# Performance work log

Hardware: AMD Instinct MI355X
Metric: run time of the kernel (lower is better)

## Reference

```python
import jax, jax.numpy as jnp
import numpy as np

HEAD_DIM = 256
V_DIM = 256
HIDDEN = 1024
SCALE_BASE = 512
GAMMA = 0.96875
BATCH, SEQ = 4, 4096


def _dup_interleave(m):
    # (L, d/2) -> (L, d), duplicating each column consecutively
    return jnp.repeat(m, 2, axis=-1)


def _rotate_every_two(x):
    x1 = x[..., ::2]
    x2 = x[..., 1::2]
    return jnp.stack([-x2, x1], axis=-1).reshape(x.shape)


def _xpos(x, downscale=False):
    # x: (B, L, head_dim); offset=0 path of XPOS.forward
    B, L, Dh = x.shape
    half = Dh // 2
    scale_buf = (jnp.arange(0, Dh, 2, dtype=jnp.float32) + 0.4 * Dh) / (1.4 * Dh)  # (half,)
    pos = jnpp = jnp.arange(L, dtype=jnp.float32)
    scale = scale_buf[None, :] ** (pos / SCALE_BASE)[:, None]  # (L, half)
    inv_freq = 1.0 / (10000.0 ** (jnp.arange(half, dtype=jnp.float32) / half))
    sinusoid = pos[:, None] * inv_freq[None, :]  # (L, half)
    sin, cos = jnp.sin(sinusoid), jnp.cos(sinusoid)
    if downscale:
        scale = 1.0 / scale
    cos_s = _dup_interleave(cos * scale)  # (L, Dh)
    sin_s = _dup_interleave(sin * scale)
    return x * cos_s[None] + _rotate_every_two(x) * sin_s[None]


def _decay_matrix(L):
    n = jnp.arange(L)[:, None]
    m = jnp.arange(L)[None, :]
    mask = n >= m
    expo = jnp.where(mask, n - m, 0).astype(jnp.float32)
    return jnp.where(mask, GAMMA ** expo, 0.0)  # (L, L)


def setup_inputs() -> dict:
    key = jax.random.key(0)
    k1, k2, k3, k4 = jax.random.split(key, 4)
    X = jax.random.normal(k1, (BATCH, SEQ, HIDDEN), dtype=jnp.float32)
    W_Q = jax.random.normal(k2, (HIDDEN, HEAD_DIM), dtype=jnp.float32) / HIDDEN
    W_K = jax.random.normal(k3, (HIDDEN, HEAD_DIM), dtype=jnp.float32) / HIDDEN
    W_V = jax.random.normal(k4, (HIDDEN, V_DIM), dtype=jnp.float32) / HIDDEN
    return {"X": X, "W_Q": W_Q, "W_K": W_K, "W_V": W_V}


def reference(X, W_Q, W_K, W_V):
    L = X.shape[1]
    Q = _xpos(X @ W_Q)                      # (B, L, Dh)
    K = _xpos(X @ W_K, downscale=True)      # (B, L, Dh)
    V = X @ W_V                             # (B, L, Dv)
    D = _decay_matrix(L)                    # (L, L)
    ret = jnp.einsum('bqd,bkd->bqk', Q, K) * D[None]  # (B, L, L)
    return ret @ V                          # (B, L, Dv)
```

## Files before the change

### kernel.cpp

```cpp
#include <hip/hip_runtime.h>
#include <hip/hip_bf16.h>
#include <cstdint>
#include <cstddef>

#define L_SEQ 4096
#define BATCH_N 4
#define HID 1024
#define DH 256
#define LOG2_GAMMA (-0.045803689613124953f)
#define INV_GAMMA32 (2.7620582f)

typedef __attribute__((ext_vector_type(8))) short short8;
typedef __attribute__((ext_vector_type(4))) float floatx4;

__device__ __forceinline__ unsigned short f2bf(float f) {
    union { float f; unsigned int u; } v; v.f = f;
    unsigned int r = (v.u + 0x7FFFu + ((v.u >> 16) & 1u)) >> 16;
    return (unsigned short)r;
}

__device__ __forceinline__ void async_copy16(const unsigned short* gsrc,
                                             unsigned short* lds) {
    __builtin_amdgcn_global_load_lds(
        (const __attribute__((address_space(1))) unsigned int*)gsrc,
        (__attribute__((address_space(3))) unsigned int*)lds, 16, 0, 0);
}

__global__ __launch_bounds__(256) void prep_kernel(
    const float* __restrict__ X, unsigned short* __restrict__ Xb,
    float2* __restrict__ tabQ, float2* __restrict__ tabK,
    const float* __restrict__ WQ, const float* __restrict__ WK,
    const float* __restrict__ WV, unsigned short* __restrict__ Wt,
    float* __restrict__ O)
{
    __shared__ float Ts[64][68];
    const int bid = blockIdx.x;
    const int t   = threadIdx.x;

    if (bid < 16384) {
        const int i = (bid * 256 + t) * 4;
        const float4 v = *(const float4*)&X[i];
        ushort4 p;
        p.x = f2bf(v.x); p.y = f2bf(v.y); p.z = f2bf(v.z); p.w = f2bf(v.w);
        *(ushort4*)&Xb[i] = p;
    } else if (bid < 18432) {
        const int gid = (bid - 16384) * 256 + t;
        const int i2  = gid >> 12;
        const int pos = gid & (L_SEQ - 1);
        const float e   = (float)pos * (1.0f / 512.0f);
        const float sb  = ((float)(2 * i2) + 102.4f) * (1.0f / 358.4f);
        const float scQ = exp2f(log2f(sb) * e);
        const float scK = 1.0f / scQ;
        const float invf = exp2f(-13.287712379549449f *
                                 ((float)i2 * (1.0f / 128.0f)));
        float s, c;
        sincosf((float)pos * invf, &s, &c);
        tabQ[gid] = make_float2(c * scQ, s * scQ);
        tabK[gid] = make_float2(c * scK, s * scK);
    } else if (bid < 18624) {
        const int idx = bid - 18432;
        const int n0 = (idx % 12) * 64;
        const int k0 = (idx / 12) * 64;
        const int seg = n0 >> 8;
        const float* __restrict__ W = (seg == 0) ? WQ : (seg == 1) ? WK : WV;
        const int nl0 = n0 & 255;

        const int r  = t >> 4;
        const int c4 = (t & 15) * 4;
        #pragma unroll
        for (int i = 0; i < 4; ++i) {
            const int kk = r + i * 16;
            const float4 v = *(const float4*)&W[(size_t)(k0 + kk) * DH + nl0 + c4];
            Ts[c4 + 0][kk] = v.x;
            Ts[c4 + 1][kk] = v.y;
            Ts[c4 + 2][kk] = v.z;
            Ts[c4 + 3][kk] = v.w;
        }
        __syncthreads();
        const int rn = t >> 3;
        const int c8 = (t & 7) * 8;
        #pragma unroll
        for (int i = 0; i < 2; ++i) {
            const int rr = rn + i * 32;
            ushort4 p0, p1;
            p0.x = f2bf(Ts[rr][c8 + 0]); p0.y = f2bf(Ts[rr][c8 + 1]);
            p0.z = f2bf(Ts[rr][c8 + 2]); p0.w = f2bf(Ts[rr][c8 + 3]);
            p1.x = f2bf(Ts[rr][c8 + 4]); p1.y = f2bf(Ts[rr][c8 + 5]);
            p1.z = f2bf(Ts[rr][c8 + 6]); p1.w = f2bf(Ts[rr][c8 + 7]);
            unsigned short* dst = &Wt[(size_t)(n0 + rr) * HID + k0 + c8];
            *(ushort4*)dst       = p0;
            *(ushort4*)(dst + 4) = p1;
        }
    } else {
        const int gid = (bid - 18624) * 256 + t;
        float4 z = (float4){0.f, 0.f, 0.f, 0.f};
        float4* dst = (float4*)O + (size_t)gid * 8;
        #pragma unroll
        for (int i = 0; i < 8; ++i) dst[i] = z;
    }
}

__global__ __launch_bounds__(256) void gemm_qkv_kernel(
    const unsigned short* __restrict__ Wt,
    const unsigned short* __restrict__ Xb,
    const float2* __restrict__ tabQ,
    const float2* __restrict__ tabK,
    unsigned short* __restrict__ Qo,
    unsigned short* __restrict__ Ko,
    unsigned short* __restrict__ VtG)
{
    __shared__ unsigned short Wa[3][128][32];
    __shared__ unsigned short Xs[3][128][32];

    const int dblk = blockIdx.x;
    const int xcd  = dblk & 7;
    const int sq   = dblk >> 3;
    const int by   = xcd * 16 + sq / 6;
    const int bx   = sq % 6;

    const int n0 = bx * 128;
    const int p0 = by * 128;
    const int t    = threadIdx.x;
    const int w    = t >> 6;
    const int lane = t & 63;
    const int quad = lane >> 4;
    const int l16  = lane & 15;
    const int wn   = (w & 1) * 64;
    const int wp   = (w >> 1) * 64;

    const int r16 = lane & 15;
    const int kq8 = (lane >> 4) * 8;

    floatx4 acc[4][4];
    #pragma unroll
    for (int i = 0; i < 4; ++i)
        #pragma unroll
        for (int j = 0; j < 4; ++j) acc[i][j] = (floatx4){0.f, 0.f, 0.f, 0.f};

    const int NT = HID / 32;

    auto stage = [&](int buf, int kt) {
        const int k0 = kt * 32;
        #pragma unroll
        for (int is = 0; is < 2; ++is) {
            const unsigned short* ga =
                &Wt[(size_t)(n0 + w * 32 + is * 16 + r16) * HID + k0 + kq8];
            const unsigned short* gb =
                &Xb[(size_t)(p0 + w * 32 + is * 16 + r16) * HID + k0 + kq8];
            async_copy16(ga, &Wa[buf][w * 32 + is * 16][0]);
            async_copy16(gb, &Xs[buf][w * 32 + is * 16][0]);
        }
    };

    stage(0, 0);
    stage(1, 1);

    for (int kt = 0; kt < NT; ++kt) {
        const int buf = kt % 3;
        if (kt + 1 < NT)
            asm volatile("s_waitcnt vmcnt(4)" ::: "memory");
        else
            asm volatile("s_waitcnt vmcnt(0)" ::: "memory");
        __builtin_amdgcn_s_barrier();

        if (kt + 2 < NT) stage((kt + 2) % 3, kt + 2);

        const char* wbp = (const char*)&Wa[buf][0][0];
        const char* xbp = (const char*)&Xs[buf][0][0];
        short8 af[4], bfv[4];
        #pragma unroll
        for (int nt = 0; nt < 4; ++nt)
            af[nt] = *(const short8*)(wbp + ((w & 1) * 4 + nt) * 1024 +
                                      quad * 256 + l16 * 16);
        #pragma unroll
        for (int pt = 0; pt < 4; ++pt)
            bfv[pt] = *(const short8*)(xbp + ((w >> 1) * 4 + pt) * 1024 +
                                       quad * 256 + l16 * 16);
        #pragma unroll
        for (int nt = 0; nt < 4; ++nt)
            #pragma unroll
            for (int pt = 0; pt < 4; ++pt)
                acc[nt][pt] = __builtin_amdgcn_mfma_f32_16x16x32_bf16(
                    af[nt], bfv[pt], acc[nt][pt], 0, 0, 0);
    }

    const int seg = n0 >> 8;
    const float2* __restrict__ tab = (seg == 1) ? tabK : tabQ;
    #pragma unroll
    for (int nt = 0; nt < 4; ++nt) {
        const int nfeat = n0 + wn + nt * 16 + quad * 4;
        const int d0 = nfeat & 255;
        #pragma unroll
        for (int pt = 0; pt < 4; ++pt) {
            const int pg  = p0 + wp + pt * 16 + l16;
            const int b   = pg >> 12;
            const int pos = pg & (L_SEQ - 1);
            if (seg == 2) {
                #pragma unroll
                for (int g = 0; g < 4; ++g)
                    VtG[(((size_t)(b * 256 + d0 + g)) << 12) + pos] =
                        f2bf(acc[nt][pt][g]);
            } else {
                float res[4];
                #pragma unroll
                for (int h = 0; h < 4; h += 2) {
                    const int i2 = (d0 + h) >> 1;
                    const float2 tc = tab[(i2 << 12) + pos];
                    const float cs = tc.x, ss = tc.y;
                    const float xe = acc[nt][pt][h], xo = acc[nt][pt][h + 1];
                    res[h]     = xe * cs - xo * ss;
                    res[h + 1] = xo * cs + xe * ss;
                }
                ushort4 pk;
                pk.x = f2bf(res[0]); pk.y = f2bf(res[1]);
                pk.z = f2bf(res[2]); pk.w = f2bf(res[3]);
                unsigned short* orow =
                    ((seg == 0) ? Qo : Ko) + (size_t)pg * DH + d0;
                *(ushort4*)orow = pk;
            }
        }
    }
}

__global__ __launch_bounds__(256) void retention_kernel(
    const unsigned short* __restrict__ Q,
    const unsigned short* __restrict__ K,
    const unsigned short* __restrict__ VtG,
    float* __restrict__ O)
{
    __shared__ short Ks[32][264];
    __shared__ short Vt[256][40];

    const int dblk = blockIdx.x;
    const int xcd  = dblk & 7;
    const int sq   = dblk >> 3;
    const int qt   = xcd * 8 + (sq & 7);
    const int b    = (sq >> 3) & 3;
    const int z    = sq >> 5;

    const int t  = threadIdx.x;
    const int q0 = qt * 64;

    const int w    = t >> 6;
    const int lane = t & 63;
    const int quad = lane >> 4;
    const int l16  = lane & 15;
    const int w16  = w * 16;

    const size_t rbase = (size_t)b * L_SEQ * DH;
    const size_t vbase = ((size_t)b * DH) << 12;

    int kst = q0 - 512; if (kst < 0) kst = 0;
    const int half32 = ((q0 + 64 - kst) >> 6) << 5;
    const int kbeg = kst + (z ? half32 : 0);
    const int kfin = z ? (q0 + 64) : (kst + half32);

    short8 qf[8];
    {
        const unsigned short* qsrc = Q + rbase + (size_t)(q0 + w16 + l16) * DH;
        #pragma unroll
        for (int dd = 0; dd < 8; ++dd)
            qf[dd] = *(const short8*)&qsrc[dd * 32 + quad * 8];
    }

    int   dint[8];
    float dec[8];
    #pragma unroll
    for (int nt = 0; nt < 2; ++nt)
        #pragma unroll
        for (int g = 0; g < 4; ++g) {
            const int idx = nt * 4 + g;
            dint[idx] = (q0 + w16 + l16) - (kbeg + nt * 16 + quad * 4 + g);
            dec[idx]  = exp2f((float)dint[idx] * LOG2_GAMMA);
        }

    floatx4 o[16];
    #pragma unroll
    for (int f = 0; f < 16; ++f) o[f] = (floatx4){0.f, 0.f, 0.f, 0.f};

    const int s0   = (quad & 1) * 2;
    const int idxA = (s0 * 16 + l16) * 4;
    const int idxB = idxA + 64;
    const bool lo  = (quad < 2);

    for (int k0 = kbeg; k0 < kfin; k0 += 32) {
        __syncthreads();
        {
            const unsigned short* src = K + rbase + (size_t)k0 * DH;
            #pragma unroll
            for (int i = 0; i < 4; ++i) {
                const int row = i * 8 + (t >> 5);
                const int col = (t & 31) * 8;
                *(uint4*)&Ks[row][col] = *(const uint4*)&src[row * DH + col];
            }
        }
        {
            const int c0   = t >> 2;
            const int koff = (t & 3) * 8;
            #pragma unroll
            for (int i = 0; i < 4; ++i) {
                const int c = c0 + 64 * i;
                *(uint4*)&Vt[c][koff] =
                    *(const uint4*)&VtG[vbase + ((size_t)c << 12) + k0 + koff];
            }
        }
        __syncthreads();

        floatx4 sA0 = (floatx4){0.f, 0.f, 0.f, 0.f};
        floatx4 sA1 = (floatx4){0.f, 0.f, 0.f, 0.f};
        floatx4 sB0 = (floatx4){0.f, 0.f, 0.f, 0.f};
        floatx4 sB1 = (floatx4){0.f, 0.f, 0.f, 0.f};
        #pragma unroll
        for (int dd = 0; dd < 4; ++dd) {
            const short8 k0f = *(const short8*)&Ks[l16][dd * 32 + quad * 8];
            const short8 k1f = *(const short8*)&Ks[16 + l16][dd * 32 + quad * 8];
            const short8 k0g = *(const short8*)&Ks[l16][(dd + 4) * 32 + quad * 8];
            const short8 k1g = *(const short8*)&Ks[16 + l16][(dd + 4) * 32 + quad * 8];
            sA0 = __builtin_amdgcn_mfma_f32_16x16x32_bf16(k0f, qf[dd], sA0, 0, 0, 0);
            sA1 = __builtin_amdgcn_mfma_f32_16x16x32_bf16(k1f, qf[dd], sA1, 0, 0, 0);
            sB0 = __builtin_amdgcn_mfma_f32_16x16x32_bf16(k0g, qf[dd + 4], sB0, 0, 0, 0);
            sB1 = __builtin_amdgcn_mfma_f32_16x16x32_bf16(k1g, qf[dd + 4], sB1, 0, 0, 0);
        }
        const floatx4 sv0 = sA0 + sB0;
        const floatx4 sv1 = sA1 + sB1;

        unsigned int pk01[2], pk23[2];
        #pragma unroll
        for (int nt = 0; nt < 2; ++nt) {
            const floatx4 sv = nt ? sv1 : sv0;
            float pv[4];
            #pragma unroll
            for (int g = 0; g < 4; ++g) {
                const int idx = nt * 4 + g;
                pv[g] = (dint[idx] >= 0) ? sv[g] * dec[idx] : 0.0f;
            }
            pk01[nt] = ((unsigned int)f2bf(pv[1]) << 16) | (unsigned int)f2bf(pv[0]);
            pk23[nt] = ((unsigned int)f2bf(pv[3]) << 16) | (unsigned int)f2bf(pv[2]);
        }
        #pragma unroll
        for (int i = 0; i < 8; ++i) { dint[i] -= 32; dec[i] *= INV_GAMMA32; }

        const int a01_0 = __builtin_amdgcn_ds_bpermute(idxA, (int)pk01[0]);
        const int a01_1 = __builtin_amdgcn_ds_bpermute(idxA, (int)pk01[1]);
        const int a23_0 = __builtin_amdgcn_ds_bpermute(idxA, (int)pk23[0]);
        const int a23_1 = __builtin_amdgcn_ds_bpermute(idxA, (int)pk23[1]);
        const int b01_0 = __builtin_amdgcn_ds_bpermute(idxB, (int)pk01[0]);
        const int b01_1 = __builtin_amdgcn_ds_bpermute(idxB, (int)pk01[1]);
        const int b23_0 = __builtin_amdgcn_ds_bpermute(idxB, (int)pk23[0]);
        const int b23_1 = __builtin_amdgcn_ds_bpermute(idxB, (int)pk23[1]);
        union { int u[4]; short8 s8; } af;
        af.u[0] = lo ? a01_0 : a01_1;
        af.u[1] = lo ? a23_0 : a23_1;
        af.u[2] = lo ? b01_0 : b01_1;
        af.u[3] = lo ? b23_0 : b23_1;

        #pragma unroll
        for (int f = 0; f < 16; ++f) {
            const short8 bfr = *(const short8*)&Vt[f * 16 + l16][quad * 8];
            o[f] = __builtin_amdgcn_mfma_f32_16x16x32_bf16(af.s8, bfr, o[f], 0, 0, 0);
        }
    }

    #pragma unroll
    for (int f = 0; f < 16; ++f) {
        #pragma unroll
        for (int g = 0; g < 4; ++g) {
            const int qpos = q0 + w16 + quad * 4 + g;
            atomicAdd(&O[rbase + (size_t)qpos * DH + f * 16 + l16], o[f][g]);
        }
    }
}

extern "C" void kernel_launch(void* const* d_in, const int* in_sizes, int n_in,
                              void* d_out, int out_size, void* d_ws, size_t ws_size,
                              hipStream_t stream)
{
    const float* X  = (const float*)d_in[0];
    const float* WQ = (const float*)d_in[1];
    const float* WK = (const float*)d_in[2];
    const float* WV = (const float*)d_in[3];
    float* out = (float*)d_out;

    const size_t per = (size_t)BATCH_N * L_SEQ * DH;
    unsigned short* Qw  = (unsigned short*)d_ws;
    unsigned short* Kw  = Qw + per;
    unsigned short* Vtw = Kw + per;
    unsigned short* Xbw = Vtw + per;
    unsigned short* Wtw = Xbw + (size_t)16384 * HID;
    float2* tabQ = (float2*)(Wtw + 786432);
    float2* tabK = tabQ + (size_t)128 * L_SEQ;

    prep_kernel<<<19136, 256, 0, stream>>>(X, Xbw, tabQ, tabK,
                                           WQ, WK, WV, Wtw, out);

    gemm_qkv_kernel<<<768, 256, 0, stream>>>(Wtw, Xbw, tabQ, tabK, Qw, Kw, Vtw);

    retention_kernel<<<512, 256, 0, stream>>>(Qw, Kw, Vtw, out);
}
```

Baseline: 213.3 us.

## Split retention work over value-dim halves and deepen QKV GEMM K-tiles with swizzle

The retention kernel now splits the value dimension between the two z-blocks instead of splitting the key range. Each block writes its 128 output columns directly, which removes the output zero-fill in prep and all fp32 atomics. The price is that each block recomputes the full QK^T scores for its key range. The QKV GEMM moves from a 3-stage 32-wide K pipeline to a 2-stage 64-wide one with an XOR-swizzled LDS layout, plus an extra barrier before the next stage is issued. This is meant to cut LDS bank conflicts and loop overhead, at some cost in load/compute overlap.

```diff
diff --git a/kernel.cpp b/kernel.cpp
--- a/kernel.cpp
+++ b/kernel.cpp
@@ -30,8 +30,7 @@
     const float* __restrict__ X, unsigned short* __restrict__ Xb,
     float2* __restrict__ tabQ, float2* __restrict__ tabK,
     const float* __restrict__ WQ, const float* __restrict__ WK,
-    const float* __restrict__ WV, unsigned short* __restrict__ Wt,
-    float* __restrict__ O)
+    const float* __restrict__ WV, unsigned short* __restrict__ Wt)
 {
     __shared__ float Ts[64][68];
     const int bid = blockIdx.x;
@@ -57,7 +56,7 @@
         sincosf((float)pos * invf, &s, &c);
         tabQ[gid] = make_float2(c * scQ, s * scQ);
         tabK[gid] = make_float2(c * scK, s * scK);
-    } else if (bid < 18624) {
+    } else {
         const int idx = bid - 18432;
         const int n0 = (idx % 12) * 64;
         const int k0 = (idx / 12) * 64;
@@ -91,12 +90,6 @@
             *(ushort4*)dst       = p0;
             *(ushort4*)(dst + 4) = p1;
         }
-    } else {
-        const int gid = (bid - 18624) * 256 + t;
-        float4 z = (float4){0.f, 0.f, 0.f, 0.f};
-        float4* dst = (float4*)O + (size_t)gid * 8;
-        #pragma unroll
-        for (int i = 0; i < 8; ++i) dst[i] = z;
     }
 }
 
@@ -109,8 +102,8 @@
     unsigned short* __restrict__ Ko,
     unsigned short* __restrict__ VtG)
 {
-    __shared__ unsigned short Wa[3][128][32];
-    __shared__ unsigned short Xs[3][128][32];
+    __shared__ unsigned short Wa[2][128][64];
+    __shared__ unsigned short Xs[2][128][64];
 
     const int dblk = blockIdx.x;
     const int xcd  = dblk & 7;
@@ -128,60 +121,69 @@
     const int wn   = (w & 1) * 64;
     const int wp   = (w >> 1) * 64;
 
-    const int r16 = lane & 15;
-    const int kq8 = (lane >> 4) * 8;
-
     floatx4 acc[4][4];
     #pragma unroll
     for (int i = 0; i < 4; ++i)
         #pragma unroll
         for (int j = 0; j < 4; ++j) acc[i][j] = (floatx4){0.f, 0.f, 0.f, 0.f};
 
-    const int NT = HID / 32;
-
+    const int NT = HID / 64;
+
+    const int g8 = lane >> 3;
+    const int pc = lane & 7;
+    const int sc = (pc ^ g8) * 8;
     auto stage = [&](int buf, int kt) {
-        const int k0 = kt * 32;
-        #pragma unroll
-        for (int is = 0; is < 2; ++is) {
+        const int k0 = kt * 64;
+        #pragma unroll
+        for (int is = 0; is < 4; ++is) {
+            const int gr = w * 8 + is * 32 + g8;
             const unsigned short* ga =
-                &Wt[(size_t)(n0 + w * 32 + is * 16 + r16) * HID + k0 + kq8];
+                &Wt[(size_t)(n0 + gr) * HID + k0 + sc];
             const unsigned short* gb =
-                &Xb[(size_t)(p0 + w * 32 + is * 16 + r16) * HID + k0 + kq8];
-            async_copy16(ga, &Wa[buf][w * 32 + is * 16][0]);
-            async_copy16(gb, &Xs[buf][w * 32 + is * 16][0]);
+                &Xb[(size_t)(p0 + gr) * HID + k0 + sc];
+            async_copy16(ga, &Wa[buf][is * 32 + w * 8][0]);
+            async_copy16(gb, &Xs[buf][is * 32 + w * 8][0]);
         }
     };
 
     stage(0, 0);
     stage(1, 1);
 
+    const int xr = l16 & 7;
+
     for (int kt = 0; kt < NT; ++kt) {
-        const int buf = kt % 3;
+        const int buf = kt & 1;
         if (kt + 1 < NT)
-            asm volatile("s_waitcnt vmcnt(4)" ::: "memory");
+            asm volatile("s_waitcnt vmcnt(8)" ::: "memory");
         else
             asm volatile("s_waitcnt vmcnt(0)" ::: "memory");
         __builtin_amdgcn_s_barrier();
 
-        if (kt + 2 < NT) stage((kt + 2) % 3, kt + 2);
-
         const char* wbp = (const char*)&Wa[buf][0][0];
         const char* xbp = (const char*)&Xs[buf][0][0];
-        short8 af[4], bfv[4];
-        #pragma unroll
-        for (int nt = 0; nt < 4; ++nt)
-            af[nt] = *(const short8*)(wbp + ((w & 1) * 4 + nt) * 1024 +
-                                      quad * 256 + l16 * 16);
-        #pragma unroll
-        for (int pt = 0; pt < 4; ++pt)
-            bfv[pt] = *(const short8*)(xbp + ((w >> 1) * 4 + pt) * 1024 +
-                                       quad * 256 + l16 * 16);
-        #pragma unroll
-        for (int nt = 0; nt < 4; ++nt)
+        short8 af[2][4], bfv[2][4];
+        #pragma unroll
+        for (int kk = 0; kk < 2; ++kk) {
+            const int pk = (((kk << 2) | quad) ^ xr) << 4;
             #pragma unroll
-            for (int pt = 0; pt < 4; ++pt)
-                acc[nt][pt] = __builtin_amdgcn_mfma_f32_16x16x32_bf16(
-                    af[nt], bfv[pt], acc[nt][pt], 0, 0, 0);
+            for (int nt = 0; nt < 4; ++nt) {
+                af[kk][nt]  = *(const short8*)(wbp + (wn + nt * 16 + l16) * 128 + pk);
+                bfv[kk][nt] = *(const short8*)(xbp + (wp + nt * 16 + l16) * 128 + pk);
+            }
+        }
+        asm volatile("s_waitcnt lgkmcnt(0)" ::: "memory");
+        __builtin_amdgcn_s_barrier();
+
+        if (kt + 2 < NT) stage(buf, kt + 2);
+
+        #pragma unroll
+        for (int kk = 0; kk < 2; ++kk)
+            #pragma unroll
+            for (int nt = 0; nt < 4; ++nt)
+                #pragma unroll
+                for (int pt = 0; pt < 4; ++pt)
+                    acc[nt][pt] = __builtin_amdgcn_mfma_f32_16x16x32_bf16(
+                        af[kk][nt], bfv[kk][pt], acc[nt][pt], 0, 0, 0);
     }
 
     const int seg = n0 >> 8;
@@ -229,7 +231,7 @@
     float* __restrict__ O)
 {
     __shared__ short Ks[32][264];
-    __shared__ short Vt[256][40];
+    __shared__ short Vt[128][40];
 
     const int dblk = blockIdx.x;
     const int xcd  = dblk & 7;
@@ -251,9 +253,7 @@
     const size_t vbase = ((size_t)b * DH) << 12;
 
     int kst = q0 - 512; if (kst < 0) kst = 0;
-    const int half32 = ((q0 + 64 - kst) >> 6) << 5;
-    const int kbeg = kst + (z ? half32 : 0);
-    const int kfin = z ? (q0 + 64) : (kst + half32);
+    const int kfin = q0 + 64;
 
     short8 qf[8];
     {
@@ -270,20 +270,20 @@
         #pragma unroll
         for (int g = 0; g < 4; ++g) {
             const int idx = nt * 4 + g;
-            dint[idx] = (q0 + w16 + l16) - (kbeg + nt * 16 + quad * 4 + g);
+            dint[idx] = (q0 + w16 + l16) - (kst + nt * 16 + quad * 4 + g);
             dec[idx]  = exp2f((float)dint[idx] * LOG2_GAMMA);
         }
 
-    floatx4 o[16];
+    floatx4 o[8];
     #pragma unroll
-    for (int f = 0; f < 16; ++f) o[f] = (floatx4){0.f, 0.f, 0.f, 0.f};
+    for (int f = 0; f < 8; ++f) o[f] = (floatx4){0.f, 0.f, 0.f, 0.f};
 
     const int s0   = (quad & 1) * 2;
     const int idxA = (s0 * 16 + l16) * 4;
     const int idxB = idxA + 64;
     const bool lo  = (quad < 2);
 
-    for (int k0 = kbeg; k0 < kfin; k0 += 32) {
+    for (int k0 = kst; k0 < kfin; k0 += 32) {
         __syncthreads();
         {
             const unsigned short* src = K + rbase + (size_t)k0 * DH;
@@ -298,10 +298,11 @@
             const int c0   = t >> 2;
             const int koff = (t & 3) * 8;
             #pragma unroll
-            for (int i = 0; i < 4; ++i) {
+            for (int i = 0; i < 2; ++i) {
                 const int c = c0 + 64 * i;
                 *(uint4*)&Vt[c][koff] =
-                    *(const uint4*)&VtG[vbase + ((size_t)c << 12) + k0 + koff];
+                    *(const uint4*)&VtG[vbase + ((size_t)(z * 128 + c) << 12) +
+                                        k0 + koff];
             }
         }
         __syncthreads();
@@ -355,18 +356,18 @@
         af.u[3] = lo ? b23_0 : b23_1;
 
         #pragma unroll
-        for (int f = 0; f < 16; ++f) {
+        for (int f = 0; f < 8; ++f) {
             const short8 bfr = *(const short8*)&Vt[f * 16 + l16][quad * 8];
             o[f] = __builtin_amdgcn_mfma_f32_16x16x32_bf16(af.s8, bfr, o[f], 0, 0, 0);
         }
     }
 
     #pragma unroll
-    for (int f = 0; f < 16; ++f) {
+    for (int f = 0; f < 8; ++f) {
         #pragma unroll
         for (int g = 0; g < 4; ++g) {
             const int qpos = q0 + w16 + quad * 4 + g;
-            atomicAdd(&O[rbase + (size_t)qpos * DH + f * 16 + l16], o[f][g]);
+            O[rbase + (size_t)qpos * DH + z * 128 + f * 16 + l16] = o[f][g];
         }
     }
 }
@@ -390,8 +391,8 @@
     float2* tabQ = (float2*)(Wtw + 786432);
     float2* tabK = tabQ + (size_t)128 * L_SEQ;
 
-    prep_kernel<<<19136, 256, 0, stream>>>(X, Xbw, tabQ, tabK,
-                                           WQ, WK, WV, Wtw, out);
+    prep_kernel<<<18624, 256, 0, stream>>>(X, Xbw, tabQ, tabK,
+                                           WQ, WK, WV, Wtw);
 
     gemm_qkv_kernel<<<768, 256, 0, stream>>>(Wtw, Xbw, tabQ, tabK, Qw, Kw, Vtw);
 
```

Measured after the change: 203.0 us. 1.05x faster.
